# Performance work log

Measured on AMD Instinct MI355X. Metric: run time of the kernel, lower is better.

## Reference

```python
import jax, jax.numpy as jnp
import numpy as np

N_NODES = 50000
N_EDGES = 800000
D_IN = 128
D_OUT = 128


def setup_inputs() -> dict:
    key = jax.random.key(0)
    ks = jax.random.split(key, 10)
    x = jax.random.normal(ks[0], (N_NODES, D_IN), dtype=jnp.float32)
    src = jax.random.randint(ks[1], (N_EDGES,), 0, N_NODES, dtype=jnp.int32)
    dst = jax.random.randint(ks[2], (N_EDGES,), 0, N_NODES, dtype=jnp.int32)
    s = 1.0 / np.sqrt(D_IN)
    def lin(k, din, dout):
        kw, kb = jax.random.split(k)
        W = jax.random.uniform(kw, (din, dout), minval=-s, maxval=s, dtype=jnp.float32)
        b = jax.random.uniform(kb, (dout,), minval=-s, maxval=s, dtype=jnp.float32)
        return W, b
    W1, b1 = lin(ks[3], D_IN, D_IN)
    W2, b2 = lin(ks[4], D_IN, D_IN)
    W3, b3 = lin(ks[5], D_IN, D_OUT)
    return dict(x=x, W1=W1, b1=b1, W2=W2, b2=b2, W3=W3, b3=b3, src=src, dst=dst)


def reference(x, W1, b1, W2, b2, W3, b3, src, dst):
    n = x.shape[0]
    ones = jnp.ones(src.shape[0], dtype=x.dtype)
    in_deg = jax.ops.segment_sum(ones, dst, num_segments=n)    # [N]
    out_deg = jax.ops.segment_sum(ones, src, num_segments=n)   # [N]

    def sage_gcn(h, W, b):
        # DGL SAGEConv(aggregator_type='gcn'), eval mode (feat_drop = identity):
        # h_neigh = (sum_{j in N(i)} h_j + h_i) / (in_deg_i + 1); out = h_neigh @ W + b
        neigh = jax.ops.segment_sum(h[src], dst, num_segments=n)  # [N, D]
        h_neigh = (neigh + h) / (in_deg + 1.0)[:, None]
        return h_neigh @ W + b

    h = sage_gcn(x, W1, b1)
    h = sage_gcn(h, W2, b2)

    # DGL GraphConv norm='both', allow_zero_in_degree=True:
    # out = D_in^{-1/2} A D_out^{-1/2} h W + b, degrees clamped to >= 1
    norm_out = jnp.clip(out_deg, 1.0) ** -0.5
    norm_in = jnp.clip(in_deg, 1.0) ** -0.5
    hs = h * norm_out[:, None]
    agg = jax.ops.segment_sum(hs[src], dst, num_segments=n)
    out = (agg * norm_in[:, None]) @ W3 + b3
    return out
```

## Files before the change

### kernel.cpp

```cpp
#include <hip/hip_runtime.h>

#define NN 50000
#define NE 800000
#define D 128

#define CH 64
#define EPC (NE / CH)
#define RG 8
#define NPR (NN / RG)

typedef short bf16x8 __attribute__((ext_vector_type(8)));
typedef float f32x4 __attribute__((ext_vector_type(4)));


__device__ __forceinline__ unsigned bf16rne(float f) {
  unsigned u = __float_as_uint(f);
  return (u + 0x7fffu + ((u >> 16) & 1u)) >> 16;
}
__device__ __forceinline__ unsigned packbf(float lo, float hi) {
  return bf16rne(lo) | (bf16rne(hi) << 16);
}

__global__ __launch_bounds__(256) void cvtw_kernel(const float* __restrict__ x,
                                                   const float* __restrict__ W1,
                                                   const float* __restrict__ W2,
                                                   const float* __restrict__ W3,
                                                   unsigned short* __restrict__ hbf,
                                                   unsigned short* __restrict__ tbl2,
                                                   unsigned short* __restrict__ T1,
                                                   unsigned short* __restrict__ T2,
                                                   unsigned short* __restrict__ T3) {
  int b = blockIdx.x;
  int tid = threadIdx.x;
  if (b < 6250) {
    int i = b * 256 + tid;
    float4 v = ((const float4*)x)[i];
    uint2 p;
    p.x = packbf(v.x, v.y);
    p.y = packbf(v.z, v.w);
    ((uint2*)hbf)[i] = p;
  } else if (b < 6442) {
    int g = b - 6250;
    int w = g >> 6;
    int i = (g & 63) * 256 + tid;
    const float* W = (w == 0) ? W1 : (w == 1) ? W2 : W3;
    unsigned short* T = (w == 0) ? T1 : (w == 1) ? T2 : T3;
    int n = i >> 7, k = i & 127;
    T[n * 128 + k] = (unsigned short)bf16rne(W[k * 128 + n]);
  } else {
    if (tid < 16) {
      ((uint4*)(hbf + (size_t)NN * D))[tid] = make_uint4(0, 0, 0, 0);
      ((uint4*)(tbl2 + (size_t)NN * D))[tid] = make_uint4(0, 0, 0, 0);
    }
  }
}

__global__ __launch_bounds__(1024) void hist_kernel(const int* __restrict__ src,
                                                    const int* __restrict__ dst,
                                                    int* __restrict__ partial_dst,
                                                    int* __restrict__ partial_src) {
  __shared__ int hd[NPR];
  __shared__ int hs[NPR];
  int tid = threadIdx.x;
  int c = blockIdx.x >> 3;
  int r = blockIdx.x & 7;
  int base = r * NPR;
  for (int i = tid; i < NPR; i += 1024) { hd[i] = 0; hs[i] = 0; }
  __syncthreads();
  int e0 = c * EPC;
  for (int i = tid; i < EPC; i += 1024) {
    int d = dst[e0 + i];
    int s = src[e0 + i];
    unsigned dr = (unsigned)(d - base);
    unsigned sr = (unsigned)(s - base);
    if (dr < NPR) atomicAdd(&hd[dr], 1);
    if (sr < NPR) atomicAdd(&hs[sr], 1);
  }
  __syncthreads();
  for (int i = tid; i < NPR; i += 1024) {
    partial_dst[c * NN + base + i] = hd[i];
    partial_src[c * NN + base + i] = hs[i];
  }
}

__device__ __forceinline__ int block_excl_scan(int v, int* wsum) {
  int lane = threadIdx.x & 63;
  int w = threadIdx.x >> 6;
  int incl = v;
#pragma unroll
  for (int off = 1; off < 64; off <<= 1) {
    int t = __shfl_up(incl, off);
    if (lane >= off) incl += t;
  }
  if (lane == 63) wsum[w] = incl;
  __syncthreads();
  int wo = 0;
#pragma unroll
  for (int j = 0; j < 4; ++j)
    if (j < w) wo += wsum[j];
  return wo + incl - v;
}

__global__ __launch_bounds__(256) void degscan_kernel(int* __restrict__ partial_dst,
                                                      const int* __restrict__ partial_src,
                                                      int* __restrict__ degtmp,
                                                      int* __restrict__ deg_out,
                                                      int* __restrict__ row_ptr,
                                                      int* __restrict__ partials, int N) {
  __shared__ int wsum[4];
  int d = blockIdx.x * 256 + threadIdx.x;
  int run = 0;
  if (d < N) {
#pragma unroll
    for (int c = 0; c < CH; ++c) {
      int v = partial_dst[c * NN + d];
      partial_dst[c * NN + d] = run;
      run += v;
    }
    degtmp[d] = run;
    int ro = 0;
#pragma unroll
    for (int c = 0; c < CH; ++c) ro += partial_src[c * NN + d];
    deg_out[d] = ro;
  }
  int pad = (run + 15) & ~15;
  int excl = block_excl_scan(pad, wsum);
  if (d < N) row_ptr[d] = excl;
  if (threadIdx.x == 255) partials[blockIdx.x] = excl + pad;
}

__global__ __launch_bounds__(256) void scan2(int* __restrict__ partials,
                                             int* __restrict__ row_ptr, int nb, int N) {
  __shared__ int wsum[4];
  int v = (threadIdx.x < nb) ? partials[threadIdx.x] : 0;
  int excl = block_excl_scan(v, wsum);
  if (threadIdx.x < nb) partials[threadIdx.x] = excl;
  if (threadIdx.x == nb - 1) row_ptr[N] = excl + v;
}

__global__ __launch_bounds__(256) void scan3(int* __restrict__ row_ptr,
                                             const int* __restrict__ partials, int N) {
  int i = blockIdx.x * 256 + threadIdx.x;
  if (i < N) row_ptr[i] += partials[blockIdx.x];
}

__global__ __launch_bounds__(1024) void fill_kernel(const int* __restrict__ src,
                                                    const int* __restrict__ dst,
                                                    const int* __restrict__ row_ptr,
                                                    const int* __restrict__ partial_dst,
                                                    const int* __restrict__ degtmp,
                                                    int* __restrict__ csr_src) {
  __shared__ int cur[NPR];
  int tid = threadIdx.x;
  int c = blockIdx.x >> 3;
  int r = blockIdx.x & 7;
  int base = r * NPR;
  for (int i = tid; i < NPR; i += 1024)
    cur[i] = row_ptr[base + i] + partial_dst[c * NN + base + i];
  if (c == 0) {
    for (int i = tid; i < NPR; i += 1024) {
      int node = base + i;
      int s = row_ptr[node] + degtmp[node];
      int e = row_ptr[node + 1];
      for (int j = s; j < e; ++j) csr_src[j] = NN;
    }
  }
  __syncthreads();
  int e0 = c * EPC;
  for (int i = tid; i < EPC; i += 1024) {
    int d = dst[e0 + i];
    unsigned dr = (unsigned)(d - base);
    if (dr < NPR) {
      int pos = atomicAdd(&cur[dr], 1);
      csr_src[pos] = src[e0 + i];
    }
  }
}

__device__ __forceinline__ void bacc(float* a, uint4 u) {
  a[0] += __uint_as_float(u.x << 16);
  a[1] += __uint_as_float(u.x & 0xffff0000u);
  a[2] += __uint_as_float(u.y << 16);
  a[3] += __uint_as_float(u.y & 0xffff0000u);
  a[4] += __uint_as_float(u.z << 16);
  a[5] += __uint_as_float(u.z & 0xffff0000u);
  a[6] += __uint_as_float(u.w << 16);
  a[7] += __uint_as_float(u.w & 0xffff0000u);
}

template <int AMODE, int GMODE, int OUT_BF>
__global__ __launch_bounds__(256) void fused_kernel(
    const unsigned short* __restrict__ hb, const int* __restrict__ row_ptr,
    const int* __restrict__ csr_src, const int* __restrict__ degtmp,
    const int* __restrict__ deg_out, const unsigned short* __restrict__ WT,
    const float* __restrict__ bias, float* __restrict__ outf,
    unsigned short* __restrict__ outb, int N) {
  __shared__ unsigned short sA[16 * 136];
  int tid = threadIdx.x;
  int wv = tid >> 6;
  int lane = tid & 63;
  int q = lane >> 4;
  int col = lane & 15;
  int base = blockIdx.x * 16;

#pragma unroll
  for (int j = 0; j < 4; ++j) {
    int jt = wv * 4 + j;
    int node = base + jt;
    int start = row_ptr[node];
    int iters = (row_ptr[node + 1] - start) >> 4;
    float a0[8] = {0, 0, 0, 0, 0, 0, 0, 0};
    float a1[8] = {0, 0, 0, 0, 0, 0, 0, 0};
    float a2[8] = {0, 0, 0, 0, 0, 0, 0, 0};
    float a3[8] = {0, 0, 0, 0, 0, 0, 0, 0};
    const int* ce = csr_src + start + q;
    for (int it = 0; it < iters; ++it, ce += 16) {
      int i0 = ce[0];
      int i1 = ce[4];
      int i2 = ce[8];
      int i3 = ce[12];
      uint4 u0 = ((const uint4*)(hb + (size_t)i0 * D))[col];
      uint4 u1 = ((const uint4*)(hb + (size_t)i1 * D))[col];
      uint4 u2 = ((const uint4*)(hb + (size_t)i2 * D))[col];
      uint4 u3 = ((const uint4*)(hb + (size_t)i3 * D))[col];
      bacc(a0, u0);
      bacc(a1, u1);
      bacc(a2, u2);
      bacc(a3, u3);
    }
#pragma unroll
    for (int t = 0; t < 8; ++t) a0[t] = (a0[t] + a1[t]) + (a2[t] + a3[t]);
#pragma unroll
    for (int t = 0; t < 8; ++t) {
      a0[t] += __shfl_xor(a0[t], 16);
      a0[t] += __shfl_xor(a0[t], 32);
    }
    int indeg = degtmp[node];
    if (AMODE == 0) {
      uint4 s = ((const uint4*)(hb + (size_t)node * D))[col];
      float sf[8] = {0, 0, 0, 0, 0, 0, 0, 0};
      bacc(sf, s);
      float inv = 1.0f / (float)(indeg + 1);
#pragma unroll
      for (int t = 0; t < 8; ++t) a0[t] = (a0[t] + sf[t]) * inv;
    } else {
      float sc = rsqrtf(fmaxf((float)indeg, 1.0f));
#pragma unroll
      for (int t = 0; t < 8; ++t) a0[t] *= sc;
    }
    if (q == 0) {
      uint4 p;
      p.x = packbf(a0[0], a0[1]);
      p.y = packbf(a0[2], a0[3]);
      p.z = packbf(a0[4], a0[5]);
      p.w = packbf(a0[6], a0[7]);
      *(uint4*)&sA[jt * 136 + col * 8] = p;
    }
  }
  __syncthreads();

  int ln = col;
  bf16x8 af[4];
#pragma unroll
  for (int c = 0; c < 4; ++c)
    af[c] = *(const bf16x8*)&sA[ln * 136 + c * 32 + q * 8];
  f32x4 acc[2];
#pragma unroll
  for (int t = 0; t < 2; ++t) acc[t] = (f32x4){0.f, 0.f, 0.f, 0.f};
#pragma unroll
  for (int t = 0; t < 2; ++t) {
    int nt = wv * 2 + t;
    const unsigned short* Wr = WT + (size_t)(nt * 16 + ln) * 128 + q * 8;
    bf16x8 b0 = *(const bf16x8*)(Wr + 0);
    bf16x8 b1 = *(const bf16x8*)(Wr + 32);
    bf16x8 b2 = *(const bf16x8*)(Wr + 64);
    bf16x8 b3 = *(const bf16x8*)(Wr + 96);
    acc[t] = __builtin_amdgcn_mfma_f32_16x16x32_bf16(af[0], b0, acc[t], 0, 0, 0);
    acc[t] = __builtin_amdgcn_mfma_f32_16x16x32_bf16(af[1], b1, acc[t], 0, 0, 0);
    acc[t] = __builtin_amdgcn_mfma_f32_16x16x32_bf16(af[2], b2, acc[t], 0, 0, 0);
    acc[t] = __builtin_amdgcn_mfma_f32_16x16x32_bf16(af[3], b3, acc[t], 0, 0, 0);
  }
  float scl[4];
#pragma unroll
  for (int r = 0; r < 4; ++r) {
    scl[r] = 1.0f;
    if (GMODE == 1) scl[r] = rsqrtf(fmaxf((float)deg_out[base + q * 4 + r], 1.0f));
  }
#pragma unroll
  for (int t = 0; t < 2; ++t) {
    int nt = wv * 2 + t;
    float b = bias[nt * 16 + ln];
#pragma unroll
    for (int r = 0; r < 4; ++r) {
      int row = base + q * 4 + r;
      float v = (acc[t][r] + b) * scl[r];
      if (OUT_BF)
        outb[(size_t)row * 128 + nt * 16 + ln] = (unsigned short)bf16rne(v);
      else
        outf[(size_t)row * 128 + nt * 16 + ln] = v;
    }
  }
}


extern "C" void kernel_launch(void* const* d_in, const int* in_sizes, int n_in,
                              void* d_out, int out_size, void* d_ws, size_t ws_size,
                              hipStream_t stream) {
  const float* x = (const float*)d_in[0];
  const float* W1 = (const float*)d_in[1];
  const float* b1 = (const float*)d_in[2];
  const float* W2 = (const float*)d_in[3];
  const float* b2 = (const float*)d_in[4];
  const float* W3 = (const float*)d_in[5];
  const float* b3 = (const float*)d_in[6];
  const int* src = (const int*)d_in[7];
  const int* dst = (const int*)d_in[8];
  float* out = (float*)d_out;

  const int N = NN;

  unsigned short* hbf = (unsigned short*)d_ws;
  unsigned short* tbl2 = hbf + (size_t)(NN + 1) * D;
  unsigned short* WT1 = tbl2 + (size_t)(NN + 1) * D;
  unsigned short* WT2 = WT1 + D * D;
  unsigned short* WT3 = WT2 + D * D;
  int* partial_dst = (int*)(WT3 + D * D);
  int* partial_src = partial_dst + (size_t)CH * NN;
  int* degtmp = partial_src + (size_t)CH * NN;
  int* deg_out = degtmp + NN;
  int* row_ptr = deg_out + NN;
  int* partials = row_ptr + NN + 1;
  int* csr_src = partials + 256;

  const int scanBlocks = (N + 255) / 256;

  cvtw_kernel<<<6443, 256, 0, stream>>>(x, W1, W2, W3, hbf, tbl2, WT1, WT2, WT3);
  hist_kernel<<<CH * RG, 1024, 0, stream>>>(src, dst, partial_dst, partial_src);
  degscan_kernel<<<scanBlocks, 256, 0, stream>>>(partial_dst, partial_src, degtmp,
                                                 deg_out, row_ptr, partials, N);
  scan2<<<1, 256, 0, stream>>>(partials, row_ptr, scanBlocks, N);
  scan3<<<scanBlocks, 256, 0, stream>>>(row_ptr, partials, N);
  fill_kernel<<<CH * RG, 1024, 0, stream>>>(src, dst, row_ptr, partial_dst, degtmp, csr_src);

  int fusedBlocks = N / 16;

  fused_kernel<0, 0, 1><<<fusedBlocks, 256, 0, stream>>>(
      hbf, row_ptr, csr_src, degtmp, deg_out, WT1, b1, nullptr, tbl2, N);
  fused_kernel<0, 1, 1><<<fusedBlocks, 256, 0, stream>>>(
      tbl2, row_ptr, csr_src, degtmp, deg_out, WT2, b2, nullptr, hbf, N);
  fused_kernel<1, 0, 0><<<fusedBlocks, 256, 0, stream>>>(
      hbf, row_ptr, csr_src, degtmp, deg_out, WT3, b3, out, nullptr, N);
}
```

Baseline: 284.6 us.

## Fuse conversion into histogram kernel and use one wave per node in fused layers

```diff
diff --git a/kernel.cpp b/kernel.cpp
--- a/kernel.cpp
+++ b/kernel.cpp
@@ -21,47 +21,41 @@
   return bf16rne(lo) | (bf16rne(hi) << 16);
 }
 
-__global__ __launch_bounds__(256) void cvtw_kernel(const float* __restrict__ x,
-                                                   const float* __restrict__ W1,
-                                                   const float* __restrict__ W2,
-                                                   const float* __restrict__ W3,
-                                                   unsigned short* __restrict__ hbf,
-                                                   unsigned short* __restrict__ tbl2,
-                                                   unsigned short* __restrict__ T1,
-                                                   unsigned short* __restrict__ T2,
-                                                   unsigned short* __restrict__ T3) {
-  int b = blockIdx.x;
+__global__ __launch_bounds__(1024) void hist_kernel(
+    const int* __restrict__ src, const int* __restrict__ dst,
+    const float* __restrict__ x, const float* __restrict__ W1,
+    const float* __restrict__ W2, const float* __restrict__ W3,
+    unsigned short* __restrict__ hbf, unsigned short* __restrict__ tbl2,
+    unsigned short* __restrict__ T1, unsigned short* __restrict__ T2,
+    unsigned short* __restrict__ T3, int* __restrict__ partial_dst,
+    int* __restrict__ partial_src) {
+  __shared__ int hd[NPR];
+  __shared__ int hs[NPR];
   int tid = threadIdx.x;
-  if (b < 6250) {
-    int i = b * 256 + tid;
+  int gid = blockIdx.x * 1024 + tid;
+
+  for (int i = gid; i < NN * D / 4; i += 512 * 1024) {
     float4 v = ((const float4*)x)[i];
     uint2 p;
     p.x = packbf(v.x, v.y);
     p.y = packbf(v.z, v.w);
     ((uint2*)hbf)[i] = p;
-  } else if (b < 6442) {
-    int g = b - 6250;
-    int w = g >> 6;
-    int i = (g & 63) * 256 + tid;
+  }
+  if (gid < 3 * 16384) {
+    int w = gid >> 14;
+    int idx = gid & 16383;
     const float* W = (w == 0) ? W1 : (w == 1) ? W2 : W3;
     unsigned short* T = (w == 0) ? T1 : (w == 1) ? T2 : T3;
-    int n = i >> 7, k = i & 127;
+    int n = idx >> 7, k = idx & 127;
     T[n * 128 + k] = (unsigned short)bf16rne(W[k * 128 + n]);
-  } else {
-    if (tid < 16) {
-      ((uint4*)(hbf + (size_t)NN * D))[tid] = make_uint4(0, 0, 0, 0);
-      ((uint4*)(tbl2 + (size_t)NN * D))[tid] = make_uint4(0, 0, 0, 0);
-    }
-  }
-}
-
-__global__ __launch_bounds__(1024) void hist_kernel(const int* __restrict__ src,
-                                                    const int* __restrict__ dst,
-                                                    int* __restrict__ partial_dst,
-                                                    int* __restrict__ partial_src) {
-  __shared__ int hd[NPR];
-  __shared__ int hs[NPR];
-  int tid = threadIdx.x;
+  } else if (gid < 3 * 16384 + 32) {
+    int z = gid - 3 * 16384;
+    if (z < 16)
+      ((uint4*)(hbf + (size_t)NN * D))[z] = make_uint4(0, 0, 0, 0);
+    else
+      ((uint4*)(tbl2 + (size_t)NN * D))[z - 16] = make_uint4(0, 0, 0, 0);
+  }
+
   int c = blockIdx.x >> 3;
   int r = blockIdx.x & 7;
   int base = r * NPR;
@@ -189,7 +183,7 @@
 }
 
 template <int AMODE, int GMODE, int OUT_BF>
-__global__ __launch_bounds__(256) void fused_kernel(
+__global__ __launch_bounds__(1024) void fused_kernel(
     const unsigned short* __restrict__ hb, const int* __restrict__ row_ptr,
     const int* __restrict__ csr_src, const int* __restrict__ degtmp,
     const int* __restrict__ deg_out, const unsigned short* __restrict__ WT,
@@ -203,10 +197,8 @@
   int col = lane & 15;
   int base = blockIdx.x * 16;
 
-#pragma unroll
-  for (int j = 0; j < 4; ++j) {
-    int jt = wv * 4 + j;
-    int node = base + jt;
+  {
+    int node = base + wv;
     int start = row_ptr[node];
     int iters = (row_ptr[node + 1] - start) >> 4;
     float a0[8] = {0, 0, 0, 0, 0, 0, 0, 0};
@@ -254,51 +246,41 @@
       p.y = packbf(a0[2], a0[3]);
       p.z = packbf(a0[4], a0[5]);
       p.w = packbf(a0[6], a0[7]);
-      *(uint4*)&sA[jt * 136 + col * 8] = p;
-    }
-  }
-  __syncthreads();
-
+      *(uint4*)&sA[wv * 136 + col * 8] = p;
+    }
+  }
+  __syncthreads();
+
+  if (wv >= 8) return;
+  int nt = wv;
   int ln = col;
   bf16x8 af[4];
 #pragma unroll
   for (int c = 0; c < 4; ++c)
     af[c] = *(const bf16x8*)&sA[ln * 136 + c * 32 + q * 8];
-  f32x4 acc[2];
-#pragma unroll
-  for (int t = 0; t < 2; ++t) acc[t] = (f32x4){0.f, 0.f, 0.f, 0.f};
-#pragma unroll
-  for (int t = 0; t < 2; ++t) {
-    int nt = wv * 2 + t;
+  f32x4 acc = (f32x4){0.f, 0.f, 0.f, 0.f};
+  {
     const unsigned short* Wr = WT + (size_t)(nt * 16 + ln) * 128 + q * 8;
     bf16x8 b0 = *(const bf16x8*)(Wr + 0);
     bf16x8 b1 = *(const bf16x8*)(Wr + 32);
     bf16x8 b2 = *(const bf16x8*)(Wr + 64);
     bf16x8 b3 = *(const bf16x8*)(Wr + 96);
-    acc[t] = __builtin_amdgcn_mfma_f32_16x16x32_bf16(af[0], b0, acc[t], 0, 0, 0);
-    acc[t] = __builtin_amdgcn_mfma_f32_16x16x32_bf16(af[1], b1, acc[t], 0, 0, 0);
-    acc[t] = __builtin_amdgcn_mfma_f32_16x16x32_bf16(af[2], b2, acc[t], 0, 0, 0);
-    acc[t] = __builtin_amdgcn_mfma_f32_16x16x32_bf16(af[3], b3, acc[t], 0, 0, 0);
-  }
-  float scl[4];
+    acc = __builtin_amdgcn_mfma_f32_16x16x32_bf16(af[0], b0, acc, 0, 0, 0);
+    acc = __builtin_amdgcn_mfma_f32_16x16x32_bf16(af[1], b1, acc, 0, 0, 0);
+    acc = __builtin_amdgcn_mfma_f32_16x16x32_bf16(af[2], b2, acc, 0, 0, 0);
+    acc = __builtin_amdgcn_mfma_f32_16x16x32_bf16(af[3], b3, acc, 0, 0, 0);
+  }
+  float b = bias[nt * 16 + ln];
 #pragma unroll
   for (int r = 0; r < 4; ++r) {
-    scl[r] = 1.0f;
-    if (GMODE == 1) scl[r] = rsqrtf(fmaxf((float)deg_out[base + q * 4 + r], 1.0f));
-  }
-#pragma unroll
-  for (int t = 0; t < 2; ++t) {
-    int nt = wv * 2 + t;
-    float b = bias[nt * 16 + ln];
-#pragma unroll
-    for (int r = 0; r < 4; ++r) {
-      int row = base + q * 4 + r;
-      float v = (acc[t][r] + b) * scl[r];
-      if (OUT_BF)
-        outb[(size_t)row * 128 + nt * 16 + ln] = (unsigned short)bf16rne(v);
-      else
-        outf[(size_t)row * 128 + nt * 16 + ln] = v;
-    }
+    int row = base + q * 4 + r;
+    float scl = 1.0f;
+    if (GMODE == 1) scl = rsqrtf(fmaxf((float)deg_out[row], 1.0f));
+    float v = (acc[r] + b) * scl;
+    if (OUT_BF)
+      outb[(size_t)row * 128 + nt * 16 + ln] = (unsigned short)bf16rne(v);
+    else
+      outf[(size_t)row * 128 + nt * 16 + ln] = v;
   }
 }
 
@@ -334,8 +316,8 @@
 
   const int scanBlocks = (N + 255) / 256;
 
-  cvtw_kernel<<<6443, 256, 0, stream>>>(x, W1, W2, W3, hbf, tbl2, WT1, WT2, WT3);
-  hist_kernel<<<CH * RG, 1024, 0, stream>>>(src, dst, partial_dst, partial_src);
+  hist_kernel<<<CH * RG, 1024, 0, stream>>>(src, dst, x, W1, W2, W3, hbf, tbl2,
+                                            WT1, WT2, WT3, partial_dst, partial_src);
   degscan_kernel<<<scanBlocks, 256, 0, stream>>>(partial_dst, partial_src, degtmp,
                                                  deg_out, row_ptr, partials, N);
   scan2<<<1, 256, 0, stream>>>(partials, row_ptr, scanBlocks, N);
@@ -344,10 +326,10 @@
 
   int fusedBlocks = N / 16;
 
-  fused_kernel<0, 0, 1><<<fusedBlocks, 256, 0, stream>>>(
+  fused_kernel<0, 0, 1><<<fusedBlocks, 1024, 0, stream>>>(
       hbf, row_ptr, csr_src, degtmp, deg_out, WT1, b1, nullptr, tbl2, N);
-  fused_kernel<0, 1, 1><<<fusedBlocks, 256, 0, stream>>>(
+  fused_kernel<0, 1, 1><<<fusedBlocks, 1024, 0, stream>>>(
       tbl2, row_ptr, csr_src, degtmp, deg_out, WT2, b2, nullptr, hbf, N);
-  fused_kernel<1, 0, 0><<<fusedBlocks, 256, 0, stream>>>(
+  fused_kernel<1, 0, 0><<<fusedBlocks, 1024, 0, stream>>>(
       hbf, row_ptr, csr_src, degtmp, deg_out, WT3, b3, out, nullptr, N);
 }
```

Measured after the change: 312.8 us. 1.1x slower.
